# Performance work log

Measured on AMD Instinct MI355X. Metric: run time of the kernel, lower is better.

The kernel has to match this reference:

```python
import jax, jax.numpy as jnp
import numpy as np

H = 16       # num_heads
D = 128      # head_dim
SCALE = 1.0 / np.sqrt(D).astype(np.float32)


def setup_inputs() -> dict:
    key = jax.random.key(0)
    ks = jax.random.split(key, 5)
    B, S, C = 2, 2048, 2048
    x = jax.random.normal(ks[0], (B, S, C), dtype=jnp.float32)
    # nn.Linear stores weight as [out_features, in_features]; scale ~ kaiming-ish
    s = 1.0 / np.sqrt(C)
    wq = jax.random.normal(ks[1], (C, C), dtype=jnp.float32) * s
    wk = jax.random.normal(ks[2], (C, C), dtype=jnp.float32) * s
    wv = jax.random.normal(ks[3], (C, C), dtype=jnp.float32) * s
    wo = jax.random.normal(ks[4], (C, C), dtype=jnp.float32) * s
    return {"x": x, "wq": wq, "wk": wk, "wv": wv, "wo": wo}


def reference(x, wq, wk, wv, wo):
    B, S, C = x.shape
    # projections: nn.Linear(x) = x @ W.T
    q = (x @ wq.T).reshape(B, S, H, D).transpose(0, 2, 1, 3)  # [B,H,S,D]
    k = (x @ wk.T).reshape(B, S, H, D).transpose(0, 2, 1, 3)
    v = (x @ wv.T).reshape(B, S, H, D).transpose(0, 2, 1, 3)
    scores = jnp.einsum('bhqd,bhkd->bhqk', q, k) * SCALE      # [B,H,S,S]
    attn = jax.nn.softmax(scores, axis=-1)
    out = jnp.einsum('bhqk,bhkd->bhqd', attn, v)              # [B,H,S,D]
    out = out.transpose(0, 2, 1, 3).reshape(B, S, H * D)
    return out @ wo.T
```

## Files before the change

### kernel.cpp

```cpp
#include <hip/hip_runtime.h>
#include <hip/hip_bf16.h>
#include <cstdint>
#include <cstddef>

typedef __bf16 bf16_t;
typedef __bf16 bf8_t __attribute__((ext_vector_type(8)));
typedef float f4_t __attribute__((ext_vector_type(4)));
typedef float f8_t __attribute__((ext_vector_type(8)));

#define DEV static __device__ __forceinline__

DEV f4_t mfma16(bf8_t a, bf8_t b, f4_t c) {
    return __builtin_amdgcn_mfma_f32_16x16x32_bf16(a, b, c, 0, 0, 0);
}

DEV bf8_t cvt8(f8_t v) {
    bf8_t r;
#pragma unroll
    for (int i = 0; i < 8; ++i) r[i] = (bf16_t)v[i];
    return r;
}

DEV void load_lds16(const bf16_t* g, bf16_t* l) {
    __builtin_amdgcn_global_load_lds(
        (const __attribute__((address_space(1))) uint32_t*)g,
        (__attribute__((address_space(3))) uint32_t*)l,
        16, 0, 0);
}

__global__ __launch_bounds__(256) void cvt_fused(const float* __restrict__ x,
                                                 const float* __restrict__ wq,
                                                 const float* __restrict__ wk,
                                                 const float* __restrict__ wv,
                                                 bf16_t* __restrict__ xb,
                                                 bf16_t* __restrict__ wqkvb) {
    const int bid = blockIdx.x;
    const float* src;
    bf16_t* dst;
    int base;
    if (bid < 4096) {
        src = x; dst = xb; base = bid;
    } else {
        const int seg = (bid - 4096) >> 11;
        src = (seg == 0) ? wq : (seg == 1) ? wk : wv;
        dst = wqkvb + (size_t)seg * 4194304;
        base = (bid - 4096) & 2047;
    }
    const size_t i = ((size_t)base * 256 + threadIdx.x) * 8;
    const f8_t v = *(const f8_t*)&src[i];
    *(bf8_t*)&dst[i] = cvt8(v);
}

__global__ __launch_bounds__(256) void cvt_bf16(const float* __restrict__ in,
                                                bf16_t* __restrict__ out, int n8) {
    const int i = blockIdx.x * 256 + threadIdx.x;
    if (i < n8) {
        const f8_t v = *(const f8_t*)&in[(size_t)i * 8];
        *(bf8_t*)&out[(size_t)i * 8] = cvt8(v);
    }
}

template <int MODE>
__global__ __launch_bounds__(256) void gemm_m97(const bf16_t* __restrict__ A,
                                                const bf16_t* __restrict__ B,
                                                void* __restrict__ C0,
                                                bf16_t* __restrict__ C1,
                                                bf16_t* __restrict__ C2,
                                                int N, int K) {
    constexpr int SMEMN = (MODE == 0) ? 128 * 136 : 8192;
    __shared__ bf16_t smem[SMEMN];
    bf16_t* As = smem;
    bf16_t* Bs = smem + 4096;

    const int tid = threadIdx.x;
    const int lane = tid & 63;
    const int wave = tid >> 6;
    const int bm0 = blockIdx.y * 128;
    const int bn0 = blockIdx.x * 128;
    const int wm = (wave >> 1) * 64;
    const int wn = (wave & 1) * 64;
    const int q4 = lane >> 4;
    const int r16 = lane & 15;

    const int srow = lane >> 2;
    const int scol = (((lane & 3) ^ ((lane >> 3) & 3))) * 8;
    const int rkey = (r16 >> 1) & 3;

    f4_t acc[4][4] = {};

    for (int k0 = 0; k0 < K; k0 += 32) {
        __syncthreads();
        load_lds16(A + (size_t)(bm0 + wave * 16 + srow) * K + k0 + scol, As + wave * 16 * 32);
        load_lds16(A + (size_t)(bm0 + 64 + wave * 16 + srow) * K + k0 + scol,
                   As + (64 + wave * 16) * 32);
        load_lds16(B + (size_t)(bn0 + wave * 16 + srow) * K + k0 + scol, Bs + wave * 16 * 32);
        load_lds16(B + (size_t)(bn0 + 64 + wave * 16 + srow) * K + k0 + scol,
                   Bs + (64 + wave * 16) * 32);
        __syncthreads();

        bf8_t af[4], bfr[4];
#pragma unroll
        for (int i = 0; i < 4; ++i)
            af[i] = *(const bf8_t*)&As[(wm + i * 16 + r16) * 32 + (q4 ^ rkey) * 8];
#pragma unroll
        for (int j = 0; j < 4; ++j)
            bfr[j] = *(const bf8_t*)&Bs[(wn + j * 16 + r16) * 32 + (q4 ^ rkey) * 8];
#pragma unroll
        for (int i = 0; i < 4; ++i)
#pragma unroll
            for (int j = 0; j < 4; ++j)
                acc[i][j] = mfma16(af[i], bfr[j], acc[i][j]);
    }

    if (MODE == 1) {
        float* C = (float*)C0;
#pragma unroll
        for (int i = 0; i < 4; ++i)
#pragma unroll
            for (int j = 0; j < 4; ++j)
#pragma unroll
                for (int r = 0; r < 4; ++r) {
                    const int m = bm0 + wm + i * 16 + q4 * 4 + r;
                    const int n = bn0 + wn + j * 16 + r16;
                    C[(size_t)m * 2048 + n] = acc[i][j][r];
                }
        return;
    }

    __syncthreads();
    if (bn0 < 4096) {
        bf16_t* dst = (bn0 < 2048) ? (bf16_t*)C0 : C1;
        const int nbase = bn0 & 2047;
#pragma unroll
        for (int i = 0; i < 4; ++i)
#pragma unroll
            for (int j = 0; j < 4; ++j)
#pragma unroll
                for (int r = 0; r < 4; ++r)
                    smem[(wm + i * 16 + q4 * 4 + r) * 136 + wn + j * 16 + r16] =
                        (bf16_t)acc[i][j][r];
        __syncthreads();
#pragma unroll
        for (int it = 0; it < 8; ++it) {
            const int idx = it * 256 + tid;
            const int m = idx >> 4;
            const int nc = (idx & 15) * 8;
            *(bf8_t*)&dst[(size_t)(bm0 + m) * 2048 + nbase + nc] =
                *(const bf8_t*)&smem[m * 136 + nc];
        }
    } else {
#pragma unroll
        for (int i = 0; i < 4; ++i)
#pragma unroll
            for (int j = 0; j < 4; ++j)
#pragma unroll
                for (int r = 0; r < 4; ++r)
                    smem[(wn + j * 16 + r16) * 136 + wm + i * 16 + q4 * 4 + r] =
                        (bf16_t)acc[i][j][r];
        __syncthreads();
        const int bb = bm0 >> 11;
        const int s0 = bm0 & 2047;
        const int nh0 = bn0 - 4096;
#pragma unroll
        for (int it = 0; it < 8; ++it) {
            const int idx = it * 256 + tid;
            const int n = idx >> 4;
            const int mc = (idx & 15) * 8;
            const bf8_t v = *(const bf8_t*)&smem[n * 136 + mc];
            const int dg = nh0 + n;
            const int h = dg >> 7, d = dg & 127;
            *(bf8_t*)&C2[(((size_t)(bb * 16 + h) * 128 + d) << 11) + s0 + mc] = v;
        }
    }
}

__global__ __launch_bounds__(256) void flash5(const bf16_t* __restrict__ Q,
                                              const bf16_t* __restrict__ K,
                                              const bf16_t* __restrict__ VT,
                                              bf16_t* __restrict__ O) {
    constexpr int S = 2048, C = 2048;
    constexpr float SCL = 0.08838834764831845f * 1.4426950408889634f;
    __shared__ bf16_t Ks[4 * 64 * 32];
    __shared__ bf16_t Vs[2 * 128 * 32];
    __shared__ bf16_t Ps[4][32 * 72];

    const int tid = threadIdx.x, lane = tid & 63, wave = tid >> 6;
    const int q4 = lane >> 4, r16 = lane & 15;
    const int bh = blockIdx.y, b = bh >> 4, h = bh & 15;
    const int q0 = blockIdx.x * 128 + wave * 32;

    const size_t qrow = (size_t)b * S + q0;
    const bf16_t* Qp0 = Q + (qrow + r16) * C + h * 128;
    const bf16_t* Qp1 = Q + (qrow + 16 + r16) * C + h * 128;
    const bf16_t* Kbase = K + (size_t)b * S * C + h * 128;
    const bf16_t* Vbase = VT + (size_t)bh * 128 * S;
    bf16_t* Pw = &Ps[wave][0];

    const int srow = lane >> 2;
    const int scol = (((lane & 3) ^ ((lane >> 3) & 3))) * 8;
    const int rkey = (r16 >> 1) & 3;

    bf8_t aq0[4], aq1[4];
#pragma unroll
    for (int kk = 0; kk < 4; ++kk) {
        aq0[kk] = *(const bf8_t*)&Qp0[kk * 32 + q4 * 8];
        aq1[kk] = *(const bf8_t*)&Qp1[kk * 32 + q4 * 8];
    }

    bf8_t ones;
#pragma unroll
    for (int i = 0; i < 8; ++i) ones[i] = (bf16_t)1.0f;

    f4_t o0[8] = {}, o1[8] = {};
    f4_t lacc0 = {}, lacc1 = {};

    for (int kv0 = 0; kv0 < S; kv0 += 64) {
        __syncthreads();
#pragma unroll
        for (int r0 = 0; r0 < 64; r0 += 16)
            load_lds16(Kbase + (size_t)(kv0 + r0 + srow) * C + wave * 32 + scol,
                       Ks + wave * 2048 + r0 * 32);
        {
            const int kkp = wave >> 1;
            const int rb = (wave & 1) * 64;
#pragma unroll
            for (int r0 = 0; r0 < 64; r0 += 16)
                load_lds16(Vbase + (size_t)(rb + r0 + srow) * S + kv0 + kkp * 32 + scol,
                           Vs + kkp * 4096 + (rb + r0) * 32);
        }
        __syncthreads();

        f4_t s4a[4] = {}, s4b[4] = {};
#pragma unroll
        for (int kk = 0; kk < 4; ++kk) {
#pragma unroll
            for (int j = 0; j < 4; ++j) {
                const bf8_t bk =
                    *(const bf8_t*)&Ks[kk * 2048 + (j * 16 + r16) * 32 + (q4 ^ rkey) * 8];
                s4a[j] = mfma16(aq0[kk], bk, s4a[j]);
                s4b[j] = mfma16(aq1[kk], bk, s4b[j]);
            }
        }

#pragma unroll
        for (int r = 0; r < 4; ++r)
#pragma unroll
            for (int j = 0; j < 4; ++j) {
                Pw[(q4 * 4 + r) * 72 + j * 16 + r16] = (bf16_t)exp2f(s4a[j][r] * SCL);
                Pw[(16 + q4 * 4 + r) * 72 + j * 16 + r16] = (bf16_t)exp2f(s4b[j][r] * SCL);
            }
        asm volatile("s_waitcnt lgkmcnt(0)" ::: "memory");

        bf8_t ap0[2], ap1[2];
#pragma unroll
        for (int kkp = 0; kkp < 2; ++kkp) {
            ap0[kkp] = *(const bf8_t*)&Pw[r16 * 72 + kkp * 32 + q4 * 8];
            ap1[kkp] = *(const bf8_t*)&Pw[(16 + r16) * 72 + kkp * 32 + q4 * 8];
        }

#pragma unroll
        for (int kkp = 0; kkp < 2; ++kkp) {
            lacc0 = mfma16(ap0[kkp], ones, lacc0);
            lacc1 = mfma16(ap1[kkp], ones, lacc1);
        }

#pragma unroll
        for (int t = 0; t < 8; ++t) {
#pragma unroll
            for (int kkp = 0; kkp < 2; ++kkp) {
                const bf8_t bv =
                    *(const bf8_t*)&Vs[kkp * 4096 + (t * 16 + r16) * 32 + (q4 ^ rkey) * 8];
                o0[t] = mfma16(ap0[kkp], bv, o0[t]);
                o1[t] = mfma16(ap1[kkp], bv, o1[t]);
            }
        }
    }

    f4_t inv0, inv1;
#pragma unroll
    for (int r = 0; r < 4; ++r) {
        inv0[r] = 1.0f / lacc0[r];
        inv1[r] = 1.0f / lacc1[r];
    }
#pragma unroll
    for (int t = 0; t < 8; ++t)
#pragma unroll
        for (int r = 0; r < 4; ++r) {
            O[(qrow + q4 * 4 + r) * C + h * 128 + t * 16 + r16] = (bf16_t)(o0[t][r] * inv0[r]);
            O[(qrow + 16 + q4 * 4 + r) * C + h * 128 + t * 16 + r16] =
                (bf16_t)(o1[t][r] * inv1[r]);
        }
}

extern "C" void kernel_launch(void* const* d_in, const int* in_sizes, int n_in,
                              void* d_out, int out_size, void* d_ws, size_t ws_size,
                              hipStream_t stream) {
    const float* x  = (const float*)d_in[0];
    const float* wq = (const float*)d_in[1];
    const float* wk = (const float*)d_in[2];
    const float* wv = (const float*)d_in[3];
    const float* wo = (const float*)d_in[4];

    bf16_t* ws = (bf16_t*)d_ws;
    bf16_t* xb   = ws;
    bf16_t* Wqkv = ws + 8388608;
    bf16_t* Qb   = ws + 20971520;
    bf16_t* Kb   = ws + 29360128;
    bf16_t* Vt   = ws + 37748736;
    bf16_t* Wob  = xb;
    bf16_t* At   = Wqkv;

    cvt_fused<<<10240, 256, 0, stream>>>(x, wq, wk, wv, xb, Wqkv);

    gemm_m97<0><<<dim3(48, 32), 256, 0, stream>>>(xb, Wqkv, Qb, Kb, Vt, 6144, 2048);

    cvt_bf16<<<2048, 256, 0, stream>>>(wo, Wob, 524288);

    flash5<<<dim3(16, 32), 256, 0, stream>>>(Qb, Kb, Vt, At);

    gemm_m97<1><<<dim3(16, 32), 256, 0, stream>>>(At, Wob, d_out, nullptr, nullptr, 2048, 2048);
}
```

Before: 431.2 us.

## Replace QKV projection GEMM with 256x256-tile, 512-thread pipelined kernel

Adds a new QKV projection GEMM that uses 256x256 output tiles with 8 waves, double-buffered LDS staging via global_load_lds, and a swizzled LDS layout. A and B k-tiles are prefetched at staggered points inside the MFMA loop, with setprio and a remapped block order for L2 locality. The epilogue stages results through LDS so Q/K are written row-major and V transposed, all with coalesced stores. The larger tiles raise arithmetic intensity, at the cost of 128KB LDS and heavy register use that limit occupancy.

```diff
diff --git a/kernel.cpp b/kernel.cpp
--- a/kernel.cpp
+++ b/kernel.cpp
@@ -60,6 +60,158 @@
     }
 }
 
+DEV void stage_half(const bf16_t* X, int row0, int rb, int kt, bf16_t* bufX,
+                    int wave, int srow, int scol) {
+#pragma unroll
+    for (int kk = 0; kk < 2; ++kk)
+        load_lds16(X + (size_t)(row0 + rb + wave * 16 + srow) * 2048 + kt * 64 + kk * 32 + scol,
+                   bufX + kk * 8192 + (rb + wave * 16) * 32);
+}
+
+__global__ __launch_bounds__(512, 2) void gemm256(const bf16_t* __restrict__ A,
+                                                  const bf16_t* __restrict__ B,
+                                                  bf16_t* __restrict__ Cq,
+                                                  bf16_t* __restrict__ Ck,
+                                                  bf16_t* __restrict__ Cv) {
+    __shared__ bf16_t smem[65536];
+
+    const int tid = threadIdx.x, lane = tid & 63, wave = tid >> 6;
+    const int wr = wave >> 2, wc = wave & 3;
+    const int q4 = lane >> 4, r16 = lane & 15;
+    const int srow = lane >> 2;
+    const int scol = ((lane & 3) ^ ((lane >> 3) & 3)) * 8;
+    const int rkey = (r16 >> 1) & 3;
+
+    int wg = blockIdx.y * 24 + blockIdx.x;
+    wg = (wg & 7) * 48 + (wg >> 3);
+    const int bm0 = (wg / 24) * 256;
+    const int bn0 = (wg % 24) * 256;
+
+    f4_t acc[8][4] = {};
+
+    {
+        bf16_t* b0 = smem;
+        bf16_t* b1 = smem + 32768;
+        stage_half(A, bm0, 0,   0, b0,          wave, srow, scol);
+        stage_half(A, bm0, 128, 0, b0,          wave, srow, scol);
+        stage_half(B, bn0, 0,   0, b0 + 16384,  wave, srow, scol);
+        stage_half(B, bn0, 128, 0, b0 + 16384,  wave, srow, scol);
+        stage_half(B, bn0, 0,   1, b1 + 16384,  wave, srow, scol);
+        stage_half(B, bn0, 128, 1, b1 + 16384,  wave, srow, scol);
+        asm volatile("s_waitcnt vmcnt(4)" ::: "memory");
+        __builtin_amdgcn_s_barrier();
+    }
+
+    for (int t = 0; t < 32; ++t) {
+        bf16_t* buf  = smem + (t & 1) * 32768;
+        bf16_t* bufN = smem + ((t + 1) & 1) * 32768;
+
+        bf8_t bq[4][2];
+#pragma unroll
+        for (int p = 0; p < 4; ++p) {
+            if (p == 0) {
+#pragma unroll
+                for (int n = 0; n < 4; ++n)
+#pragma unroll
+                    for (int kk = 0; kk < 2; ++kk)
+                        bq[n][kk] = *(const bf8_t*)&buf[16384 + kk * 8192 +
+                                                       (wc * 64 + n * 16 + r16) * 32 +
+                                                       (q4 ^ rkey) * 8];
+            }
+            bf8_t af[2][2];
+#pragma unroll
+            for (int i = 0; i < 2; ++i)
+#pragma unroll
+                for (int kk = 0; kk < 2; ++kk)
+                    af[i][kk] = *(const bf8_t*)&buf[kk * 8192 +
+                                                    (wr * 128 + (2 * p + i) * 16 + r16) * 32 +
+                                                    (q4 ^ rkey) * 8];
+
+            if (p == 0 && t + 1 < 32) {
+                stage_half(A, bm0, 0,   t + 1, bufN, wave, srow, scol);
+                stage_half(A, bm0, 128, t + 1, bufN, wave, srow, scol);
+            }
+            if (p == 1 && t + 2 < 32)
+                stage_half(B, bn0, 0,   t + 2, buf + 16384, wave, srow, scol);
+            if (p == 2 && t + 2 < 32)
+                stage_half(B, bn0, 128, t + 2, buf + 16384, wave, srow, scol);
+
+            __builtin_amdgcn_s_barrier();
+            asm volatile("s_waitcnt lgkmcnt(0)" ::: "memory");
+            __builtin_amdgcn_s_setprio(1);
+#pragma unroll
+            for (int kk = 0; kk < 2; ++kk)
+#pragma unroll
+                for (int i = 0; i < 2; ++i)
+#pragma unroll
+                    for (int n = 0; n < 4; ++n)
+                        acc[2 * p + i][n] = mfma16(af[i][kk], bq[n][kk], acc[2 * p + i][n]);
+            __builtin_amdgcn_s_setprio(0);
+            if (p == 3) {
+                if (t < 30) {
+                    asm volatile("s_waitcnt vmcnt(4)" ::: "memory");
+                } else {
+                    asm volatile("s_waitcnt vmcnt(0)" ::: "memory");
+                }
+            }
+            __builtin_amdgcn_s_barrier();
+        }
+    }
+
+    __syncthreads();
+
+    bf16_t* strip = smem + wave * 4608;
+    if (bn0 < 4096) {
+        bf16_t* dst = (bn0 < 2048) ? Cq : Ck;
+        const int nb = (bn0 & 2047) + wc * 64;
+#pragma unroll
+        for (int P = 0; P < 2; ++P) {
+#pragma unroll
+            for (int i = 0; i < 4; ++i)
+#pragma unroll
+                for (int n = 0; n < 4; ++n)
+#pragma unroll
+                    for (int r = 0; r < 4; ++r)
+                        strip[(i * 16 + q4 * 4 + r) * 72 + n * 16 + r16] =
+                            (bf16_t)acc[P * 4 + i][n][r];
+            asm volatile("s_waitcnt lgkmcnt(0)" ::: "memory");
+#pragma unroll
+            for (int it = 0; it < 8; ++it) {
+                const int row = it * 8 + (lane >> 3);
+                const int c = (lane & 7) * 8;
+                *(bf8_t*)&dst[(size_t)(bm0 + wr * 128 + P * 64 + row) * 2048 + nb + c] =
+                    *(const bf8_t*)&strip[row * 72 + c];
+            }
+            asm volatile("s_waitcnt lgkmcnt(0)" ::: "memory");
+        }
+    } else {
+        const int bb = bm0 >> 11;
+        const int s0 = bm0 & 2047;
+#pragma unroll
+        for (int P = 0; P < 2; ++P) {
+#pragma unroll
+            for (int i = 0; i < 4; ++i)
+#pragma unroll
+                for (int n = 0; n < 4; ++n)
+#pragma unroll
+                    for (int r = 0; r < 4; ++r)
+                        strip[(n * 16 + r16) * 72 + i * 16 + q4 * 4 + r] =
+                            (bf16_t)acc[P * 4 + i][n][r];
+            asm volatile("s_waitcnt lgkmcnt(0)" ::: "memory");
+#pragma unroll
+            for (int it = 0; it < 8; ++it) {
+                const int nrow = it * 8 + (lane >> 3);
+                const int c = (lane & 7) * 8;
+                const int dg = (bn0 - 4096) + wc * 64 + nrow;
+                const int h = dg >> 7, d = dg & 127;
+                *(bf8_t*)&Cv[(((size_t)(bb * 16 + h) * 128 + d) << 11) + s0 + wr * 128 + P * 64 + c] =
+                    *(const bf8_t*)&strip[nrow * 72 + c];
+            }
+            asm volatile("s_waitcnt lgkmcnt(0)" ::: "memory");
+        }
+    }
+}
+
 template <int MODE>
 __global__ __launch_bounds__(256) void gemm_m97(const bf16_t* __restrict__ A,
                                                 const bf16_t* __restrict__ B,
@@ -312,7 +464,7 @@
 
     cvt_fused<<<10240, 256, 0, stream>>>(x, wq, wk, wv, xb, Wqkv);
 
-    gemm_m97<0><<<dim3(48, 32), 256, 0, stream>>>(xb, Wqkv, Qb, Kb, Vt, 6144, 2048);
+    gemm256<<<dim3(24, 16), 512, 0, stream>>>(xb, Wqkv, Qb, Kb, Vt);
 
     cvt_bf16<<<2048, 256, 0, stream>>>(wo, Wob, 524288);
 
```

Measured after the change: 412.5 us. -4.3%, faster.
